# Kernel optimization log

Measured on AMD Instinct MI355X. Metric: run time of the kernel, lower is better.

## Reference

```python
import jax, jax.numpy as jnp
import numpy as np

DIM = 256
WINDOW = 8
HEADS = 8
N = WINDOW * WINDOW


def _make_rpb_index(window_size: int) -> jnp.ndarray:
    hs = np.arange(window_size)
    coords = np.stack(np.meshgrid(hs, hs, indexing='ij'))  # [2, w, w]
    flat = coords.reshape(2, -1)                            # [2, N]
    rel = flat[:, :, None] - flat[:, None, :]               # [2, N, N]
    rel = rel.transpose(1, 2, 0).copy()                     # [N, N, 2]
    rel[:, :, 0] += window_size - 1
    rel[:, :, 1] += window_size - 1
    rel[:, :, 0] *= 2 * window_size - 1
    return jnp.asarray(rel.sum(-1), dtype=jnp.int32)        # [N, N]


def setup_inputs() -> dict:
    key = jax.random.key(0)
    k_x, k_qw, k_qb, k_pw, k_pb, k_rpb = jax.random.split(key, 6)
    B_ = 2048
    x = jax.random.normal(k_x, (B_, N, DIM), dtype=jnp.float32)
    mask = jnp.zeros((64, N, N), dtype=jnp.float32)
    # nn.Linear weights stored [out, in] as in torch
    qkv_w = jax.random.normal(k_qw, (3 * DIM, DIM), dtype=jnp.float32) * 0.02
    qkv_b = jnp.zeros((3 * DIM,), dtype=jnp.float32)
    proj_w = jax.random.normal(k_pw, (DIM, DIM), dtype=jnp.float32) * 0.02
    proj_b = jnp.zeros((DIM,), dtype=jnp.float32)
    rpb_table = jax.random.normal(k_rpb, ((2 * WINDOW - 1) ** 2, HEADS), dtype=jnp.float32) * 0.02
    rpb_index = _make_rpb_index(WINDOW)
    return {"x": x, "mask": mask, "qkv_w": qkv_w, "qkv_b": qkv_b,
            "proj_w": proj_w, "proj_b": proj_b, "rpb_table": rpb_table,
            "rpb_index": rpb_index}


def reference(x, mask, qkv_w, qkv_b, proj_w, proj_b, rpb_table, rpb_index):
    B_, n, C = x.shape
    H = HEADS
    d = C // H
    scale = d ** -0.5
    qkv = x @ qkv_w.T + qkv_b                      # [B, N, 3C]
    qkv = qkv.reshape(B_, n, 3, H, d)
    q = qkv[:, :, 0].transpose(0, 2, 1, 3)          # [B, H, N, d]
    k = qkv[:, :, 1].transpose(0, 2, 1, 3)
    v = qkv[:, :, 2].transpose(0, 2, 1, 3)
    attn = jnp.einsum('bhnd,bhmd->bhnm', q * scale, k)
    rpb = rpb_table[rpb_index]                      # [N, N, H]
    attn = attn + rpb.transpose(2, 0, 1)[None]      # [B, H, N, N]
    nW = mask.shape[0]
    attn = attn.reshape(B_ // nW, nW, H, n, n) + mask[None, :, None]
    attn = attn.reshape(B_, H, n, n)
    attn = jax.nn.softmax(attn, axis=-1)
    out = jnp.einsum('bhnm,bhmd->bhnd', attn, v)    # [B, H, N, d]
    out = out.transpose(0, 2, 1, 3).reshape(B_, n, C)
    return out @ proj_w.T + proj_b
```

## Files before the change

### kernel.cpp

```cpp
#include <hip/hip_runtime.h>
#include <hip/hip_bf16.h>


#define TOK 64
#define CDIM 256
#define SCRB 32768
#define AT   32768

typedef __attribute__((ext_vector_type(8))) short short8;
typedef __attribute__((ext_vector_type(4))) float f32x4;
typedef __attribute__((ext_vector_type(4))) float float4_t;

__device__ __forceinline__ short f2bf(float f) {
  union { float f; unsigned u; } v; v.f = f;
  unsigned r = v.u + 0x7FFFu + ((v.u >> 16) & 1u);
  return (short)(r >> 16);
}

__device__ __forceinline__ unsigned cvt2(float a, float b) {
  union { __hip_bfloat162 h; unsigned u; } v;
  v.h = __float22bfloat162_rn(make_float2(a, b));
  return v.u;
}

__device__ __forceinline__ short8 pack88(f32x4 lo, f32x4 hi) {
  union { short8 s; unsigned u[4]; } r;
  r.u[0] = cvt2(lo[0], lo[1]);
  r.u[1] = cvt2(lo[2], lo[3]);
  r.u[2] = cvt2(hi[0], hi[1]);
  r.u[3] = cvt2(hi[2], hi[3]);
  return r.s;
}

__device__ __forceinline__ int rm_addr(int base, int row, int col) {
  return base + row * 512 + ((col * 2) ^ ((row & 7) << 4));
}

__global__ void preconv_kernel(const float* __restrict__ qkv_w,
                               const float* __restrict__ proj_w,
                               const float* __restrict__ rpb_table,
                               const int* __restrict__ rpb_index,
                               const float* __restrict__ mask,
                               short* __restrict__ wqkv,
                               short* __restrict__ wproj,
                               float* __restrict__ rpbT,
                               float* __restrict__ maskT) {
  int idx = blockIdx.x * blockDim.x + threadIdx.x;
  const float scale = 0.17677669529663687f;
  const int NW1 = 768 * 256;
  const int NW2 = NW1 + 256 * 256;
  const int NW3 = NW2 + 8 * 64 * 64;
  const int NW4 = NW3 + 64 * 64 * 64;
  if (idx < NW1) {
    float v = qkv_w[idx];
    if (idx < 256 * 256) v *= scale;
    wqkv[idx] = f2bf(v);
  } else if (idx < NW2) {
    int i = idx - NW1;
    wproj[i] = f2bf(proj_w[i]);
  } else if (idx < NW3) {
    int i = idx - NW2;
    int h = i >> 12;
    int pos = i & 4095;
    int qtok = pos >> 6;
    int t = pos & 63;
    int llv = t >> 2, ni = t & 3;
    int kt = ni * 16 + llv;
    rpbT[i] = rpb_table[rpb_index[qtok * 64 + kt] * 8 + h];
  } else if (idx < NW4) {
    int i = idx - NW3;
    int win = i >> 12;
    int pos = i & 4095;
    int qtok = pos >> 6;
    int t = pos & 63;
    int llv = t >> 2, ni = t & 3;
    int kt = ni * 16 + llv;
    maskT[i] = mask[win * 4096 + qtok * 64 + kt];
  }
}

__global__ void __launch_bounds__(512) fused_attn(
    const float* __restrict__ x, const float* __restrict__ qkv_b,
    const float* __restrict__ proj_b,
    const short* __restrict__ wqkv, const short* __restrict__ wproj,
    const float* __restrict__ rpbT, const float* __restrict__ maskT,
    float* __restrict__ out) {
  extern __shared__ char smem[];
  const int b = blockIdx.x;
  const int tid = threadIdx.x;
  const int w = tid >> 6;
  const int lane = tid & 63;
  const int lg = lane >> 4;
  const int ll = lane & 15;
  const float scale = 0.17677669529663687f;
  const int S0 = SCRB + w * 8192;
  const int S1 = S0 + 4096;

  {
    const int row = tid >> 3;
    const int c0 = (tid & 7) * 32;
    const float4_t* src = reinterpret_cast<const float4_t*>(
        x + (size_t)b * TOK * CDIM + row * CDIM + c0);
#pragma unroll
    for (int j = 0; j < 4; ++j) {
      float4_t f0 = src[2 * j];
      float4_t f1 = src[2 * j + 1];
      *reinterpret_cast<short8*>(smem + rm_addr(0, row, c0 + 8 * j)) =
          pack88(f0, f1);
    }
  }
  __syncthreads();

  f32x4 aqk[4][4] = {};
#pragma unroll
  for (int ks = 0; ks < 8; ++ks) {
    const int k0 = ks * 32 + lg * 8;
    short8 xf[4];
#pragma unroll
    for (int ni = 0; ni < 4; ++ni)
      xf[ni] = *reinterpret_cast<const short8*>(smem + rm_addr(0, ni * 16 + ll, k0));
#pragma unroll
    for (int j = 0; j < 4; ++j) {
      const int cbase = (j >> 1) * 256 + w * 32 + (j & 1) * 16;
      short8 wf = *reinterpret_cast<const short8*>(wqkv + (cbase + ll) * 256 + k0);
#pragma unroll
      for (int ni = 0; ni < 4; ++ni)
        aqk[ni][j] = __builtin_amdgcn_mfma_f32_16x16x32_bf16(wf, xf[ni], aqk[ni][j], 0, 0, 0);
    }
  }
  f32x4 bj[4];
#pragma unroll
  for (int j = 0; j < 4; ++j) {
    float4_t t = *reinterpret_cast<const float4_t*>(
        qkv_b + (j >> 1) * 256 + w * 32 + (j & 1) * 16 + lg * 4);
    bj[j] = (j < 2) ? t * scale : t;
  }
  short8 aq[4], bk[4];
#pragma unroll
  for (int ni = 0; ni < 4; ++ni) {
    aq[ni] = pack88(aqk[ni][0] + bj[0], aqk[ni][1] + bj[1]);
    bk[ni] = pack88(aqk[ni][2] + bj[2], aqk[ni][3] + bj[3]);
  }

  f32x4 av[4][2] = {};
#pragma unroll
  for (int ks = 0; ks < 8; ++ks) {
    const int k0 = ks * 32 + lg * 8;
    short8 xf[4];
#pragma unroll
    for (int mi = 0; mi < 4; ++mi)
      xf[mi] = *reinterpret_cast<const short8*>(smem + rm_addr(0, mi * 16 + ll, k0));
#pragma unroll
    for (int hf = 0; hf < 2; ++hf) {
      short8 wfv = *reinterpret_cast<const short8*>(
          wqkv + (512 + w * 32 + hf * 16 + ll) * 256 + k0);
#pragma unroll
      for (int mi = 0; mi < 4; ++mi)
        av[mi][hf] = __builtin_amdgcn_mfma_f32_16x16x32_bf16(xf[mi], wfv, av[mi][hf], 0, 0, 0);
    }
  }
#pragma unroll
  for (int hf = 0; hf < 2; ++hf) {
    float bb = qkv_b[512 + w * 32 + hf * 16 + ll];
    int d = hf * 16 + ll;
#pragma unroll
    for (int mi = 0; mi < 4; ++mi) {
      f32x4 v = av[mi][hf];
      int tok0 = 16 * mi + lg * 4;
      union { unsigned long long q; unsigned u[2]; } pk;
      pk.u[0] = cvt2(v[0] + bb, v[1] + bb);
      pk.u[1] = cvt2(v[2] + bb, v[3] + bb);
      *reinterpret_cast<unsigned long long*>(
          smem + S0 + d * 128 + ((tok0 * 2) ^ ((d & 7) << 4))) = pk.q;
    }
  }

  f32x4 sa[4][4];
  {
    f32x4 z{0.0f, 0.0f, 0.0f, 0.0f};
#pragma unroll
    for (int mi = 0; mi < 4; ++mi)
#pragma unroll
      for (int ni = 0; ni < 4; ++ni)
        sa[mi][ni] = __builtin_amdgcn_mfma_f32_16x16x32_bf16(aq[mi], bk[ni], z, 0, 0, 0);
    const float4_t* rpT4 = reinterpret_cast<const float4_t*>(rpbT) + w * 1024;
    const float4_t* mkT4 = reinterpret_cast<const float4_t*>(maskT) + (b & 63) * 1024;
#pragma unroll
    for (int mi = 0; mi < 4; ++mi)
#pragma unroll
      for (int r = 0; r < 4; ++r) {
        int qtok = mi * 16 + lg * 4 + r;
        float4_t f = rpT4[qtok * 16 + ll];
        float4_t g = mkT4[qtok * 16 + ll];
#pragma unroll
        for (int ni = 0; ni < 4; ++ni)
          sa[mi][ni][r] += f[ni] + g[ni];
      }
  }

  float rinv[4][4];
#pragma unroll
  for (int mi = 0; mi < 4; ++mi)
#pragma unroll
    for (int r = 0; r < 4; ++r) {
      float m = sa[mi][0][r];
#pragma unroll
      for (int ni = 1; ni < 4; ++ni) m = fmaxf(m, sa[mi][ni][r]);
      for (int d = 1; d < 16; d <<= 1) m = fmaxf(m, __shfl_xor(m, d));
      float sum = 0.f;
#pragma unroll
      for (int ni = 0; ni < 4; ++ni) {
        float e = __expf(sa[mi][ni][r] - m);
        sa[mi][ni][r] = e;
        sum += e;
      }
      for (int d = 1; d < 16; d <<= 1) sum += __shfl_xor(sum, d);
      rinv[mi][r] = 1.0f / sum;
    }

  f32x4 oa[2][4] = {};
#pragma unroll
  for (int ks = 0; ks < 2; ++ks) {
#pragma unroll
    for (int mi = 0; mi < 4; ++mi)
#pragma unroll
      for (int nio = 0; nio < 2; ++nio) {
        int ni = 2 * ks + nio;
        unsigned u01 = cvt2(sa[mi][ni][0] * rinv[mi][0], sa[mi][ni][1] * rinv[mi][1]);
        unsigned u23 = cvt2(sa[mi][ni][2] * rinv[mi][2], sa[mi][ni][3] * rinv[mi][3]);
        int col2 = (nio * 16 + ll) * 2;
        int qt0 = 16 * mi + lg * 4;
        *reinterpret_cast<short*>(smem + S1 + (qt0 + 0) * 64 + (col2 ^ (((qt0 + 0) & 3) << 4))) = (short)(u01);
        *reinterpret_cast<short*>(smem + S1 + (qt0 + 1) * 64 + (col2 ^ (((qt0 + 1) & 3) << 4))) = (short)(u01 >> 16);
        *reinterpret_cast<short*>(smem + S1 + (qt0 + 2) * 64 + (col2 ^ (((qt0 + 2) & 3) << 4))) = (short)(u23);
        *reinterpret_cast<short*>(smem + S1 + (qt0 + 3) * 64 + (col2 ^ (((qt0 + 3) & 3) << 4))) = (short)(u23 >> 16);
      }
    short8 pf[4], vf[2];
#pragma unroll
    for (int ni = 0; ni < 4; ++ni) {
      int qt = ll + 16 * ni;
      pf[ni] = *reinterpret_cast<const short8*>(
          smem + S1 + qt * 64 + ((lg * 16) ^ ((qt & 3) << 4)));
    }
#pragma unroll
    for (int hf = 0; hf < 2; ++hf) {
      int d = ll + 16 * hf;
      vf[hf] = *reinterpret_cast<const short8*>(
          smem + S0 + d * 128 + (((ks * 32 + lg * 8) * 2) ^ ((d & 7) << 4)));
    }
#pragma unroll
    for (int hf = 0; hf < 2; ++hf)
#pragma unroll
      for (int ni = 0; ni < 4; ++ni)
        oa[hf][ni] = __builtin_amdgcn_mfma_f32_16x16x32_bf16(vf[hf], pf[ni], oa[hf][ni], 0, 0, 0);
  }

  __syncthreads();

#pragma unroll
  for (int hf = 0; hf < 2; ++hf)
#pragma unroll
    for (int ni = 0; ni < 4; ++ni) {
      int qt = ll + 16 * ni;
      int ch0 = w * 32 + hf * 16 + lg * 4;
      union { unsigned long long q; unsigned u[2]; } pk;
      pk.u[0] = cvt2(oa[hf][ni][0], oa[hf][ni][1]);
      pk.u[1] = cvt2(oa[hf][ni][2], oa[hf][ni][3]);
      *reinterpret_cast<unsigned long long*>(
          smem + AT + qt * 512 + ((ch0 * 2) ^ ((qt & 7) << 4))) = pk.q;
    }
  __syncthreads();

  f32x4 pa[2][4] = {};
#pragma unroll
  for (int ks = 0; ks < 8; ++ks) {
    const int k0 = ks * 32 + lg * 8;
    short8 af[4];
#pragma unroll
    for (int ni = 0; ni < 4; ++ni)
      af[ni] = *reinterpret_cast<const short8*>(smem + rm_addr(AT, ni * 16 + ll, k0));
#pragma unroll
    for (int j = 0; j < 2; ++j) {
      short8 wf = *reinterpret_cast<const short8*>(wproj + (w * 32 + j * 16 + ll) * 256 + k0);
#pragma unroll
      for (int ni = 0; ni < 4; ++ni)
        pa[j][ni] = __builtin_amdgcn_mfma_f32_16x16x32_bf16(wf, af[ni], pa[j][ni], 0, 0, 0);
    }
  }
  float* outp = out + (size_t)b * TOK * CDIM;
#pragma unroll
  for (int j = 0; j < 2; ++j) {
    float4_t pb = *reinterpret_cast<const float4_t*>(proj_b + w * 32 + j * 16 + lg * 4);
#pragma unroll
    for (int ni = 0; ni < 4; ++ni) {
      f32x4 v = pa[j][ni] + pb;
      *reinterpret_cast<float4_t*>(outp + (ni * 16 + ll) * 256 + w * 32 + j * 16 + lg * 4) = v;
    }
  }
}

extern "C" void kernel_launch(void* const* d_in, const int* in_sizes, int n_in,
                              void* d_out, int out_size, void* d_ws, size_t ws_size,
                              hipStream_t stream) {
  const float* x        = (const float*)d_in[0];
  const float* mask     = (const float*)d_in[1];
  const float* qkv_w    = (const float*)d_in[2];
  const float* qkv_b    = (const float*)d_in[3];
  const float* proj_w   = (const float*)d_in[4];
  const float* proj_b   = (const float*)d_in[5];
  const float* rpb_tab  = (const float*)d_in[6];
  const int*   rpb_idx  = (const int*)d_in[7];
  float* out = (float*)d_out;

  short* wqkv  = (short*)d_ws;
  short* wproj = wqkv + 768 * 256;
  float* rpbT  = (float*)(wproj + 256 * 256);
  float* maskT = rpbT + 8 * 64 * 64;

  int total = 768 * 256 + 256 * 256 + 8 * 64 * 64 + 64 * 64 * 64;
  preconv_kernel<<<(total + 255) / 256, 256, 0, stream>>>(
      qkv_w, proj_w, rpb_tab, rpb_idx, mask, wqkv, wproj, rpbT, maskT);

  hipFuncSetAttribute((const void*)fused_attn,
                      hipFuncAttributeMaxDynamicSharedMemorySize, 98304);
  int B = in_sizes[0] / (TOK * CDIM);
  fused_attn<<<B, 512, 98304, stream>>>(x, qkv_b, proj_b, wqkv, wproj,
                                        rpbT, maskT, out);
}
```

Measured before the change: 248.6 us.

## Split fused attention into per-head wave kernels plus separate projection kernel

Replaces the one-block-per-window fused kernel (512 threads, 96KB LDS) with a per-(window, head) single-wave attention kernel that reads fp32 x directly from global memory. The attention output is staged as bf16 in the output buffer. A second kernel then runs the output projection from that buffer. Block indices are swizzled so blocks that share a window are spread across groups. The aim is to raise occupancy and remove block-wide barriers and the large LDS footprint. In exchange, each head wave re-reads all of x (8x redundant global traffic, though much of it should hit cache), the kernel pays a global round trip for the intermediate, and it adds one more launch.

```diff
diff --git a/kernel.cpp b/kernel.cpp
--- a/kernel.cpp
+++ b/kernel.cpp
@@ -4,8 +4,6 @@
 
 #define TOK 64
 #define CDIM 256
-#define SCRB 32768
-#define AT   32768
 
 typedef __attribute__((ext_vector_type(8))) short short8;
 typedef __attribute__((ext_vector_type(4))) float f32x4;
@@ -30,10 +28,6 @@
   r.u[2] = cvt2(hi[0], hi[1]);
   r.u[3] = cvt2(hi[2], hi[3]);
   return r.s;
-}
-
-__device__ __forceinline__ int rm_addr(int base, int row, int col) {
-  return base + row * 512 + ((col * 2) ^ ((row & 7) << 4));
 }
 
 __global__ void preconv_kernel(const float* __restrict__ qkv_w,
@@ -79,37 +73,22 @@
   }
 }
 
-__global__ void __launch_bounds__(512) fused_attn(
+__global__ void __launch_bounds__(64, 3) attn_kernel(
     const float* __restrict__ x, const float* __restrict__ qkv_b,
-    const float* __restrict__ proj_b,
-    const short* __restrict__ wqkv, const short* __restrict__ wproj,
+    const short* __restrict__ wqkv,
     const float* __restrict__ rpbT, const float* __restrict__ maskT,
     float* __restrict__ out) {
-  extern __shared__ char smem[];
-  const int b = blockIdx.x;
-  const int tid = threadIdx.x;
-  const int w = tid >> 6;
-  const int lane = tid & 63;
+  __shared__ char smem[8192];
+  const int bid = blockIdx.x;
+  const int sid = (bid & 7) * 2048 + (bid >> 3);
+  const int w = sid >> 3;
+  const int h = sid & 7;
+  const int lane = threadIdx.x & 63;
   const int lg = lane >> 4;
   const int ll = lane & 15;
   const float scale = 0.17677669529663687f;
-  const int S0 = SCRB + w * 8192;
-  const int S1 = S0 + 4096;
-
-  {
-    const int row = tid >> 3;
-    const int c0 = (tid & 7) * 32;
-    const float4_t* src = reinterpret_cast<const float4_t*>(
-        x + (size_t)b * TOK * CDIM + row * CDIM + c0);
-#pragma unroll
-    for (int j = 0; j < 4; ++j) {
-      float4_t f0 = src[2 * j];
-      float4_t f1 = src[2 * j + 1];
-      *reinterpret_cast<short8*>(smem + rm_addr(0, row, c0 + 8 * j)) =
-          pack88(f0, f1);
-    }
-  }
-  __syncthreads();
+
+  const float* xb = x + (size_t)w * TOK * CDIM;
 
   f32x4 aqk[4][4] = {};
 #pragma unroll
@@ -117,11 +96,14 @@
     const int k0 = ks * 32 + lg * 8;
     short8 xf[4];
 #pragma unroll
-    for (int ni = 0; ni < 4; ++ni)
-      xf[ni] = *reinterpret_cast<const short8*>(smem + rm_addr(0, ni * 16 + ll, k0));
+    for (int ni = 0; ni < 4; ++ni) {
+      const float* px = xb + (ni * 16 + ll) * 256 + k0;
+      xf[ni] = pack88(*reinterpret_cast<const float4_t*>(px),
+                      *reinterpret_cast<const float4_t*>(px + 4));
+    }
 #pragma unroll
     for (int j = 0; j < 4; ++j) {
-      const int cbase = (j >> 1) * 256 + w * 32 + (j & 1) * 16;
+      const int cbase = (j >> 1) * 256 + h * 32 + (j & 1) * 16;
       short8 wf = *reinterpret_cast<const short8*>(wqkv + (cbase + ll) * 256 + k0);
 #pragma unroll
       for (int ni = 0; ni < 4; ++ni)
@@ -132,7 +114,7 @@
 #pragma unroll
   for (int j = 0; j < 4; ++j) {
     float4_t t = *reinterpret_cast<const float4_t*>(
-        qkv_b + (j >> 1) * 256 + w * 32 + (j & 1) * 16 + lg * 4);
+        qkv_b + (j >> 1) * 256 + h * 32 + (j & 1) * 16 + lg * 4);
     bj[j] = (j < 2) ? t * scale : t;
   }
   short8 aq[4], bk[4];
@@ -148,12 +130,15 @@
     const int k0 = ks * 32 + lg * 8;
     short8 xf[4];
 #pragma unroll
-    for (int mi = 0; mi < 4; ++mi)
-      xf[mi] = *reinterpret_cast<const short8*>(smem + rm_addr(0, mi * 16 + ll, k0));
+    for (int mi = 0; mi < 4; ++mi) {
+      const float* px = xb + (mi * 16 + ll) * 256 + k0;
+      xf[mi] = pack88(*reinterpret_cast<const float4_t*>(px),
+                      *reinterpret_cast<const float4_t*>(px + 4));
+    }
 #pragma unroll
     for (int hf = 0; hf < 2; ++hf) {
       short8 wfv = *reinterpret_cast<const short8*>(
-          wqkv + (512 + w * 32 + hf * 16 + ll) * 256 + k0);
+          wqkv + (512 + h * 32 + hf * 16 + ll) * 256 + k0);
 #pragma unroll
       for (int mi = 0; mi < 4; ++mi)
         av[mi][hf] = __builtin_amdgcn_mfma_f32_16x16x32_bf16(xf[mi], wfv, av[mi][hf], 0, 0, 0);
@@ -161,7 +146,7 @@
   }
 #pragma unroll
   for (int hf = 0; hf < 2; ++hf) {
-    float bb = qkv_b[512 + w * 32 + hf * 16 + ll];
+    float bb = qkv_b[512 + h * 32 + hf * 16 + ll];
     int d = hf * 16 + ll;
 #pragma unroll
     for (int mi = 0; mi < 4; ++mi) {
@@ -171,7 +156,7 @@
       pk.u[0] = cvt2(v[0] + bb, v[1] + bb);
       pk.u[1] = cvt2(v[2] + bb, v[3] + bb);
       *reinterpret_cast<unsigned long long*>(
-          smem + S0 + d * 128 + ((tok0 * 2) ^ ((d & 7) << 4))) = pk.q;
+          smem + d * 128 + ((tok0 * 2) ^ ((d & 7) << 4))) = pk.q;
     }
   }
 
@@ -183,8 +168,8 @@
 #pragma unroll
       for (int ni = 0; ni < 4; ++ni)
         sa[mi][ni] = __builtin_amdgcn_mfma_f32_16x16x32_bf16(aq[mi], bk[ni], z, 0, 0, 0);
-    const float4_t* rpT4 = reinterpret_cast<const float4_t*>(rpbT) + w * 1024;
-    const float4_t* mkT4 = reinterpret_cast<const float4_t*>(maskT) + (b & 63) * 1024;
+    const float4_t* rpT4 = reinterpret_cast<const float4_t*>(rpbT) + h * 1024;
+    const float4_t* mkT4 = reinterpret_cast<const float4_t*>(maskT) + (w & 63) * 1024;
 #pragma unroll
     for (int mi = 0; mi < 4; ++mi)
 #pragma unroll
@@ -230,23 +215,23 @@
         unsigned u23 = cvt2(sa[mi][ni][2] * rinv[mi][2], sa[mi][ni][3] * rinv[mi][3]);
         int col2 = (nio * 16 + ll) * 2;
         int qt0 = 16 * mi + lg * 4;
-        *reinterpret_cast<short*>(smem + S1 + (qt0 + 0) * 64 + (col2 ^ (((qt0 + 0) & 3) << 4))) = (short)(u01);
-        *reinterpret_cast<short*>(smem + S1 + (qt0 + 1) * 64 + (col2 ^ (((qt0 + 1) & 3) << 4))) = (short)(u01 >> 16);
-        *reinterpret_cast<short*>(smem + S1 + (qt0 + 2) * 64 + (col2 ^ (((qt0 + 2) & 3) << 4))) = (short)(u23);
-        *reinterpret_cast<short*>(smem + S1 + (qt0 + 3) * 64 + (col2 ^ (((qt0 + 3) & 3) << 4))) = (short)(u23 >> 16);
+        *reinterpret_cast<short*>(smem + 4096 + (qt0 + 0) * 64 + (col2 ^ (((qt0 + 0) & 3) << 4))) = (short)(u01);
+        *reinterpret_cast<short*>(smem + 4096 + (qt0 + 1) * 64 + (col2 ^ (((qt0 + 1) & 3) << 4))) = (short)(u01 >> 16);
+        *reinterpret_cast<short*>(smem + 4096 + (qt0 + 2) * 64 + (col2 ^ (((qt0 + 2) & 3) << 4))) = (short)(u23);
+        *reinterpret_cast<short*>(smem + 4096 + (qt0 + 3) * 64 + (col2 ^ (((qt0 + 3) & 3) << 4))) = (short)(u23 >> 16);
       }
     short8 pf[4], vf[2];
 #pragma unroll
     for (int ni = 0; ni < 4; ++ni) {
       int qt = ll + 16 * ni;
       pf[ni] = *reinterpret_cast<const short8*>(
-          smem + S1 + qt * 64 + ((lg * 16) ^ ((qt & 3) << 4)));
+          smem + 4096 + qt * 64 + ((lg * 16) ^ ((qt & 3) << 4)));
     }
 #pragma unroll
     for (int hf = 0; hf < 2; ++hf) {
       int d = ll + 16 * hf;
       vf[hf] = *reinterpret_cast<const short8*>(
-          smem + S0 + d * 128 + (((ks * 32 + lg * 8) * 2) ^ ((d & 7) << 4)));
+          smem + d * 128 + (((ks * 32 + lg * 8) * 2) ^ ((d & 7) << 4)));
     }
 #pragma unroll
     for (int hf = 0; hf < 2; ++hf)
@@ -255,46 +240,60 @@
         oa[hf][ni] = __builtin_amdgcn_mfma_f32_16x16x32_bf16(vf[hf], pf[ni], oa[hf][ni], 0, 0, 0);
   }
 
-  __syncthreads();
-
+  char* ob = reinterpret_cast<char*>(out) + (size_t)w * TOK * 1024;
 #pragma unroll
   for (int hf = 0; hf < 2; ++hf)
 #pragma unroll
     for (int ni = 0; ni < 4; ++ni) {
       int qt = ll + 16 * ni;
-      int ch0 = w * 32 + hf * 16 + lg * 4;
       union { unsigned long long q; unsigned u[2]; } pk;
       pk.u[0] = cvt2(oa[hf][ni][0], oa[hf][ni][1]);
       pk.u[1] = cvt2(oa[hf][ni][2], oa[hf][ni][3]);
       *reinterpret_cast<unsigned long long*>(
-          smem + AT + qt * 512 + ((ch0 * 2) ^ ((qt & 7) << 4))) = pk.q;
-    }
-  __syncthreads();
-
-  f32x4 pa[2][4] = {};
+          ob + (size_t)qt * 1024 + h * 64 + hf * 32 + lg * 8) = pk.q;
+    }
+}
+
+__global__ void __launch_bounds__(256, 3) proj_kernel(
+    const short* __restrict__ wproj, const float* __restrict__ proj_b,
+    float* __restrict__ out) {
+  const int bid = blockIdx.x;
+  const int t = (bid & 7) * 256 + (bid >> 3);
+  const int wv = threadIdx.x >> 6;
+  const int lane = threadIdx.x & 63;
+  const int lg = lane >> 4;
+  const int ll = lane & 15;
+  const char* ab = reinterpret_cast<const char*>(out) + (size_t)t * TOK * 1024;
+
+  f32x4 pa[4][4] = {};
 #pragma unroll
   for (int ks = 0; ks < 8; ++ks) {
     const int k0 = ks * 32 + lg * 8;
     short8 af[4];
 #pragma unroll
     for (int ni = 0; ni < 4; ++ni)
-      af[ni] = *reinterpret_cast<const short8*>(smem + rm_addr(AT, ni * 16 + ll, k0));
-#pragma unroll
-    for (int j = 0; j < 2; ++j) {
-      short8 wf = *reinterpret_cast<const short8*>(wproj + (w * 32 + j * 16 + ll) * 256 + k0);
+      af[ni] = *reinterpret_cast<const short8*>(
+          ab + (size_t)(ni * 16 + ll) * 1024 + k0 * 2);
+#pragma unroll
+    for (int jj = 0; jj < 4; ++jj) {
+      short8 wf = *reinterpret_cast<const short8*>(
+          wproj + (wv * 64 + jj * 16 + ll) * 256 + k0);
 #pragma unroll
       for (int ni = 0; ni < 4; ++ni)
-        pa[j][ni] = __builtin_amdgcn_mfma_f32_16x16x32_bf16(wf, af[ni], pa[j][ni], 0, 0, 0);
-    }
-  }
-  float* outp = out + (size_t)b * TOK * CDIM;
-#pragma unroll
-  for (int j = 0; j < 2; ++j) {
-    float4_t pb = *reinterpret_cast<const float4_t*>(proj_b + w * 32 + j * 16 + lg * 4);
+        pa[jj][ni] = __builtin_amdgcn_mfma_f32_16x16x32_bf16(wf, af[ni], pa[jj][ni], 0, 0, 0);
+    }
+  }
+  __syncthreads();
+
+  float* op = out + (size_t)t * TOK * CDIM;
+#pragma unroll
+  for (int jj = 0; jj < 4; ++jj) {
+    int oc0 = wv * 64 + jj * 16 + lg * 4;
+    float4_t pb = *reinterpret_cast<const float4_t*>(proj_b + oc0);
 #pragma unroll
     for (int ni = 0; ni < 4; ++ni) {
-      f32x4 v = pa[j][ni] + pb;
-      *reinterpret_cast<float4_t*>(outp + (ni * 16 + ll) * 256 + w * 32 + j * 16 + lg * 4) = v;
+      f32x4 v = pa[jj][ni] + pb;
+      *reinterpret_cast<float4_t*>(op + (ni * 16 + ll) * 256 + oc0) = v;
     }
   }
 }
@@ -321,9 +320,7 @@
   preconv_kernel<<<(total + 255) / 256, 256, 0, stream>>>(
       qkv_w, proj_w, rpb_tab, rpb_idx, mask, wqkv, wproj, rpbT, maskT);
 
-  hipFuncSetAttribute((const void*)fused_attn,
-                      hipFuncAttributeMaxDynamicSharedMemorySize, 98304);
   int B = in_sizes[0] / (TOK * CDIM);
-  fused_attn<<<B, 512, 98304, stream>>>(x, qkv_b, proj_b, wqkv, wproj,
-                                        rpbT, maskT, out);
-}
+  attn_kernel<<<B * 8, 64, 0, stream>>>(x, qkv_b, wqkv, rpbT, maskT, out);
+  proj_kernel<<<B, 256, 0, stream>>>(wproj, proj_b, out);
+}
```

Result: slower. 463.7 us (+86.5%).
